# Performance work log

Hardware: AMD Instinct MI355X
Metric: run time of the kernel (lower is better)

Reference implementation:

```python
import jax, jax.numpy as jnp
import numpy as np

N_NODES = 50000
N_EDGES = 1600000
EMB_DIM = 128
HIDDEN = 128   # 2 * out_channels
OUT = 64       # out_channels


def setup_inputs() -> dict:
    key = jax.random.key(0)
    ks = jax.random.split(key, 8)
    x = jnp.arange(N_NODES, dtype=jnp.int64)
    edge_index = jax.random.randint(ks[0], (2, N_EDGES), 0, N_NODES, dtype=jnp.int64)
    emb = jax.random.normal(ks[1], (N_NODES, EMB_DIM), dtype=jnp.float32) * 0.02
    W1 = jax.random.normal(ks[2], (EMB_DIM, HIDDEN), dtype=jnp.float32) / np.sqrt(EMB_DIM).astype(np.float32)
    b1 = jax.random.normal(ks[3], (HIDDEN,), dtype=jnp.float32) * 0.01
    W_mu = jax.random.normal(ks[4], (HIDDEN, OUT), dtype=jnp.float32) / np.sqrt(HIDDEN).astype(np.float32)
    b_mu = jax.random.normal(ks[5], (OUT,), dtype=jnp.float32) * 0.01
    W_logvar = jax.random.normal(ks[6], (HIDDEN, OUT), dtype=jnp.float32) / np.sqrt(HIDDEN).astype(np.float32)
    b_logvar = jax.random.normal(ks[7], (OUT,), dtype=jnp.float32) * 0.01
    return {"x": x, "edge_index": edge_index, "emb": emb, "W1": W1, "b1": b1,
            "W_mu": W_mu, "b_mu": b_mu, "W_logvar": W_logvar, "b_logvar": b_logvar}


def _gcn_norm(edge_index, n_nodes):
    # PyG GCNConv default: add self-loops, symmetric normalization D^-1/2 A D^-1/2
    row, col = edge_index[0], edge_index[1]
    loop = jnp.arange(n_nodes, dtype=row.dtype)
    row = jnp.concatenate([row, loop])  # source nodes
    col = jnp.concatenate([col, loop])  # target nodes (aggregation index)
    deg = jax.ops.segment_sum(jnp.ones_like(col, dtype=jnp.float32), col, num_segments=n_nodes)
    dis = jnp.where(deg > 0, jax.lax.rsqrt(jnp.maximum(deg, 1.0)), 0.0)
    norm = dis[row] * dis[col]  # [E + N]
    return row, col, norm


def _gcn_conv(h, row, col, norm, W, b, n_nodes):
    h = h @ W                               # [N, out]
    msg = h[row] * norm[:, None]            # gather source feats, scale per edge
    out = jax.ops.segment_sum(msg, col, num_segments=n_nodes)  # scatter-add at targets
    return out + b


def reference(x, edge_index, emb, W1, b1, W_mu, b_mu, W_logvar, b_logvar):
    n_nodes = emb.shape[0]
    row, col, norm = _gcn_norm(edge_index, n_nodes)
    h = emb[x]                                                  # embedding lookup
    h = jax.nn.relu(_gcn_conv(h, row, col, norm, W1, b1, n_nodes))
    mu = _gcn_conv(h, row, col, norm, W_mu, b_mu, n_nodes)
    logvar = _gcn_conv(h, row, col, norm, W_logvar, b_logvar, n_nodes)
    return (mu, logvar)
```

## Files before the change

kernel.cpp:

```cpp
#include <hip/hip_runtime.h>
#include <hip/hip_bf16.h>

typedef unsigned int uint32;


__global__ __launch_bounds__(256)
void zero_cnt_kernel(uint32* __restrict__ cnt, int n) {
    int i = blockIdx.x * 256 + threadIdx.x;
    if (i < n) cnt[i] = 0u;
}

__global__ __launch_bounds__(256)
void count_kernel(const int* __restrict__ col, int n_edges, uint32* __restrict__ cnt) {
    int e = blockIdx.x * 256 + threadIdx.x;
    if (e < n_edges) atomicAdd(&cnt[col[e]], 1u);
}

__global__ __launch_bounds__(256)
void scan_blk_kernel(const uint32* __restrict__ cnt, uint32* __restrict__ partial,
                     uint32* __restrict__ blk_sums, int n) {
    __shared__ uint32 sh[256];
    int i = blockIdx.x * 256 + (int)threadIdx.x;
    uint32 v = (i < n) ? cnt[i] : 0u;
    sh[threadIdx.x] = v;
    __syncthreads();
    for (int off = 1; off < 256; off <<= 1) {
        uint32 t = (threadIdx.x >= (unsigned)off) ? sh[threadIdx.x - off] : 0u;
        __syncthreads();
        sh[threadIdx.x] += t;
        __syncthreads();
    }
    if (i < n) partial[i] = sh[threadIdx.x] - v;
    if (threadIdx.x == 255) blk_sums[blockIdx.x] = sh[255];
}

__global__ __launch_bounds__(1024)
void scan_sums_kernel(const uint32* __restrict__ blk_sums, uint32* __restrict__ blk_offs, int nb) {
    __shared__ uint32 sh[1024];
    uint32 v = ((int)threadIdx.x < nb) ? blk_sums[threadIdx.x] : 0u;
    sh[threadIdx.x] = v;
    __syncthreads();
    for (int off = 1; off < 1024; off <<= 1) {
        uint32 t = (threadIdx.x >= (unsigned)off) ? sh[threadIdx.x - off] : 0u;
        __syncthreads();
        sh[threadIdx.x] += t;
        __syncthreads();
    }
    if ((int)threadIdx.x < nb) blk_offs[threadIdx.x] = sh[threadIdx.x] - v;
}

__global__ __launch_bounds__(256)
void scan_add_kernel(const uint32* __restrict__ partial, const uint32* __restrict__ blk_offs,
                     const uint32* __restrict__ cnt, uint32* __restrict__ offs,
                     float* __restrict__ dis, uint32* __restrict__ cursor,
                     int n, int n_edges) {
    int i = blockIdx.x * 256 + (int)threadIdx.x;
    if (i < n) {
        offs[i] = partial[i] + blk_offs[blockIdx.x];
        dis[i] = rsqrtf((float)(cnt[i] + 1u));
        cursor[i] = 0u;
    }
    if (i == 0) offs[n] = (uint32)n_edges;
}

__global__ __launch_bounds__(256)
void fill_kernel(const int* __restrict__ row, const int* __restrict__ col, int n_edges,
                 const uint32* __restrict__ offs, uint32* __restrict__ cursor,
                 uint32* __restrict__ csr) {
    int e = blockIdx.x * 256 + threadIdx.x;
    if (e < n_edges) {
        int c = col[e];
        uint32 p = offs[c] + atomicAdd(&cursor[c], 1u);
        csr[p] = (uint32)row[e];
    }
}

static __device__ __forceinline__ uint32 f32_to_bf16_rne(float f) {
    uint32 u = __float_as_uint(f);
    return (u + 0x7fffu + ((u >> 16) & 1u)) >> 16;
}
static __device__ __forceinline__ float bf16_lo(uint32 v) {
    return __uint_as_float(v << 16);
}
static __device__ __forceinline__ float bf16_hi(uint32 v) {
    return __uint_as_float(v & 0xffff0000u);
}

__global__ __launch_bounds__(256)
void gemm_scale_kernel(const float* __restrict__ A, const int* __restrict__ gather,
                       const float* __restrict__ W0, const float* __restrict__ W1b,
                       int wstride, const float* __restrict__ dis,
                       uint32* __restrict__ out, int n_rows) {
    int grp = threadIdx.x >> 4;
    int c8  = (threadIdx.x & 15) * 8;
    int r0  = blockIdx.x * 64 + grp * 4;
    if (r0 >= n_rows) return;

    const float* wb = (c8 < 64) ? (W0 + c8) : (W1b + (c8 - 64));

    const float* ap[4];
    #pragma unroll
    for (int i = 0; i < 4; i++) {
        int r = r0 + i;
        if (r > n_rows - 1) r = n_rows - 1;
        int ra = gather ? gather[r] : r;
        ap[i] = A + (size_t)ra * 128;
    }

    float acc[4][8];
    #pragma unroll
    for (int i = 0; i < 4; i++)
        #pragma unroll
        for (int j = 0; j < 8; j++) acc[i][j] = 0.f;

    for (int k = 0; k < 128; k += 4) {
        float4 av[4];
        #pragma unroll
        for (int i = 0; i < 4; i++) av[i] = *(const float4*)(ap[i] + k);

        const float* w = wb + (size_t)k * wstride;
        #pragma unroll
        for (int kk = 0; kk < 4; kk++) {
            float4 w0 = *(const float4*)(w);
            float4 w1 = *(const float4*)(w + 4);
            #pragma unroll
            for (int i = 0; i < 4; i++) {
                float s = (kk == 0) ? av[i].x : (kk == 1) ? av[i].y
                        : (kk == 2) ? av[i].z : av[i].w;
                acc[i][0] = fmaf(s, w0.x, acc[i][0]);
                acc[i][1] = fmaf(s, w0.y, acc[i][1]);
                acc[i][2] = fmaf(s, w0.z, acc[i][2]);
                acc[i][3] = fmaf(s, w0.w, acc[i][3]);
                acc[i][4] = fmaf(s, w1.x, acc[i][4]);
                acc[i][5] = fmaf(s, w1.y, acc[i][5]);
                acc[i][6] = fmaf(s, w1.z, acc[i][6]);
                acc[i][7] = fmaf(s, w1.w, acc[i][7]);
            }
            w += wstride;
        }
    }

    #pragma unroll
    for (int i = 0; i < 4; i++) {
        int r = r0 + i;
        if (r < n_rows) {
            float d = dis[r];
            uint4 pk;
            pk.x = f32_to_bf16_rne(d * acc[i][0]) | (f32_to_bf16_rne(d * acc[i][1]) << 16);
            pk.y = f32_to_bf16_rne(d * acc[i][2]) | (f32_to_bf16_rne(d * acc[i][3]) << 16);
            pk.z = f32_to_bf16_rne(d * acc[i][4]) | (f32_to_bf16_rne(d * acc[i][5]) << 16);
            pk.w = f32_to_bf16_rne(d * acc[i][6]) | (f32_to_bf16_rne(d * acc[i][7]) << 16);
            *(uint4*)(out + (size_t)r * 64 + (c8 >> 1)) = pk;
        }
    }
}

__global__ __launch_bounds__(256)
void agg_relu_kernel(const uint32* __restrict__ hs, const uint32* __restrict__ offs,
                     const uint32* __restrict__ csr, const float* __restrict__ dis,
                     const float* __restrict__ bias, float* __restrict__ out, int n_nodes) {
    int wid = (blockIdx.x * 256 + (int)threadIdx.x) >> 6;
    int lane = threadIdx.x & 63;
    if (wid >= n_nodes) return;

    uint32 sv = hs[(size_t)wid * 64 + lane];
    float ax = bf16_lo(sv), ay = bf16_hi(sv);
    int beg = (int)offs[wid], end = (int)offs[wid + 1];

    int j = beg;
    for (; j + 8 <= end; j += 8) {
        uint32 e0 = csr[j],     e1 = csr[j + 1], e2 = csr[j + 2], e3 = csr[j + 3];
        uint32 e4 = csr[j + 4], e5 = csr[j + 5], e6 = csr[j + 6], e7 = csr[j + 7];
        uint32 v0 = hs[(size_t)e0 * 64 + lane];
        uint32 v1 = hs[(size_t)e1 * 64 + lane];
        uint32 v2 = hs[(size_t)e2 * 64 + lane];
        uint32 v3 = hs[(size_t)e3 * 64 + lane];
        uint32 v4 = hs[(size_t)e4 * 64 + lane];
        uint32 v5 = hs[(size_t)e5 * 64 + lane];
        uint32 v6 = hs[(size_t)e6 * 64 + lane];
        uint32 v7 = hs[(size_t)e7 * 64 + lane];
        float sx = ((bf16_lo(v0) + bf16_lo(v1)) + (bf16_lo(v2) + bf16_lo(v3)))
                 + ((bf16_lo(v4) + bf16_lo(v5)) + (bf16_lo(v6) + bf16_lo(v7)));
        float sy = ((bf16_hi(v0) + bf16_hi(v1)) + (bf16_hi(v2) + bf16_hi(v3)))
                 + ((bf16_hi(v4) + bf16_hi(v5)) + (bf16_hi(v6) + bf16_hi(v7)));
        ax += sx; ay += sy;
    }
    for (; j < end; ++j) {
        uint32 v = hs[(size_t)csr[j] * 64 + lane];
        ax += bf16_lo(v); ay += bf16_hi(v);
    }

    float d = dis[wid];
    float2 b = ((const float2*)bias)[lane];
    float2 o;
    o.x = fmaxf(fmaf(d, ax, b.x), 0.f);
    o.y = fmaxf(fmaf(d, ay, b.y), 0.f);
    ((float2*)out)[(size_t)wid * 64 + lane] = o;
}

__global__ __launch_bounds__(256)
void agg_out_kernel(const uint32* __restrict__ hs, const uint32* __restrict__ offs,
                    const uint32* __restrict__ csr, const float* __restrict__ dis,
                    const float* __restrict__ bmu, const float* __restrict__ blv,
                    float* __restrict__ out_mu, float* __restrict__ out_lv, int n_nodes) {
    int wid = (blockIdx.x * 256 + (int)threadIdx.x) >> 6;
    int lane = threadIdx.x & 63;
    if (wid >= n_nodes) return;

    uint32 sv = hs[(size_t)wid * 64 + lane];
    float ax = bf16_lo(sv), ay = bf16_hi(sv);
    int beg = (int)offs[wid], end = (int)offs[wid + 1];

    int j = beg;
    for (; j + 8 <= end; j += 8) {
        uint32 e0 = csr[j],     e1 = csr[j + 1], e2 = csr[j + 2], e3 = csr[j + 3];
        uint32 e4 = csr[j + 4], e5 = csr[j + 5], e6 = csr[j + 6], e7 = csr[j + 7];
        uint32 v0 = hs[(size_t)e0 * 64 + lane];
        uint32 v1 = hs[(size_t)e1 * 64 + lane];
        uint32 v2 = hs[(size_t)e2 * 64 + lane];
        uint32 v3 = hs[(size_t)e3 * 64 + lane];
        uint32 v4 = hs[(size_t)e4 * 64 + lane];
        uint32 v5 = hs[(size_t)e5 * 64 + lane];
        uint32 v6 = hs[(size_t)e6 * 64 + lane];
        uint32 v7 = hs[(size_t)e7 * 64 + lane];
        float sx = ((bf16_lo(v0) + bf16_lo(v1)) + (bf16_lo(v2) + bf16_lo(v3)))
                 + ((bf16_lo(v4) + bf16_lo(v5)) + (bf16_lo(v6) + bf16_lo(v7)));
        float sy = ((bf16_hi(v0) + bf16_hi(v1)) + (bf16_hi(v2) + bf16_hi(v3)))
                 + ((bf16_hi(v4) + bf16_hi(v5)) + (bf16_hi(v6) + bf16_hi(v7)));
        ax += sx; ay += sy;
    }
    for (; j < end; ++j) {
        uint32 v = hs[(size_t)csr[j] * 64 + lane];
        ax += bf16_lo(v); ay += bf16_hi(v);
    }

    float d = dis[wid];
    if (lane < 32) {
        float2 b = ((const float2*)bmu)[lane];
        float2 o = make_float2(fmaf(d, ax, b.x), fmaf(d, ay, b.y));
        ((float2*)out_mu)[(size_t)wid * 32 + lane] = o;
    } else {
        int l2 = lane - 32;
        float2 b = ((const float2*)blv)[l2];
        float2 o = make_float2(fmaf(d, ax, b.x), fmaf(d, ay, b.y));
        ((float2*)out_lv)[(size_t)wid * 32 + l2] = o;
    }
}


extern "C" void kernel_launch(void* const* d_in, const int* in_sizes, int n_in,
                              void* d_out, int out_size, void* d_ws, size_t ws_size,
                              hipStream_t stream) {
    const int*   x   = (const int*)d_in[0];
    const int*   ei  = (const int*)d_in[1];
    const float* emb = (const float*)d_in[2];
    const float* W1  = (const float*)d_in[3];
    const float* b1  = (const float*)d_in[4];
    const float* Wmu = (const float*)d_in[5];
    const float* bmu = (const float*)d_in[6];
    const float* Wlv = (const float*)d_in[7];
    const float* blv = (const float*)d_in[8];

    int n_nodes = in_sizes[0];
    int n_edges = in_sizes[1] / 2;
    const int* row = ei;
    const int* col = ei + n_edges;

    char* wp = (char*)d_ws;
    auto carve = [&wp](size_t bytes) -> char* {
        char* p = wp;
        wp += (bytes + 255) & ~(size_t)255;
        return p;
    };
    int nb = (n_nodes + 255) / 256;

    uint32* cnt     = (uint32*)carve((size_t)n_nodes * 4);
    uint32* cursor  = (uint32*)carve((size_t)n_nodes * 4);
    uint32* offs    = (uint32*)carve(((size_t)n_nodes + 1) * 4);
    uint32* partial = (uint32*)carve((size_t)n_nodes * 4);
    uint32* bsums   = (uint32*)carve((size_t)nb * 4);
    uint32* boffs   = (uint32*)carve((size_t)nb * 4);
    float*  dis     = (float*) carve((size_t)n_nodes * 4);
    uint32* csr     = (uint32*)carve((size_t)n_edges * 4);
    uint32* bufA    = (uint32*)carve((size_t)n_nodes * 64 * 4);
    float*  bufB    = (float*) carve((size_t)n_nodes * 128 * 4);

    int gb_e = (n_edges + 255) / 256;

    hipLaunchKernelGGL(zero_cnt_kernel, dim3(nb), dim3(256), 0, stream, cnt, n_nodes);
    hipLaunchKernelGGL(count_kernel, dim3(gb_e), dim3(256), 0, stream, col, n_edges, cnt);
    hipLaunchKernelGGL(scan_blk_kernel, dim3(nb), dim3(256), 0, stream, cnt, partial, bsums, n_nodes);
    hipLaunchKernelGGL(scan_sums_kernel, dim3(1), dim3(1024), 0, stream, bsums, boffs, nb);
    hipLaunchKernelGGL(scan_add_kernel, dim3(nb), dim3(256), 0, stream,
                       partial, boffs, cnt, offs, dis, cursor, n_nodes, n_edges);
    hipLaunchKernelGGL(fill_kernel, dim3(gb_e), dim3(256), 0, stream, row, col, n_edges, offs, cursor, csr);

    int gemm_blocks = (n_nodes + 63) / 64;
    int agg_blocks  = (n_nodes + 3) / 4;

    hipLaunchKernelGGL(gemm_scale_kernel, dim3(gemm_blocks), dim3(256), 0, stream,
                       emb, x, W1, W1 + 64, 128, dis, bufA, n_nodes);
    hipLaunchKernelGGL(agg_relu_kernel, dim3(agg_blocks), dim3(256), 0, stream,
                       bufA, offs, csr, dis, b1, bufB, n_nodes);

    hipLaunchKernelGGL(gemm_scale_kernel, dim3(gemm_blocks), dim3(256), 0, stream,
                       bufB, (const int*)nullptr, Wmu, Wlv, 64, dis, bufA, n_nodes);

    float* out_mu = (float*)d_out;
    float* out_lv = out_mu + (size_t)n_nodes * 64;
    hipLaunchKernelGGL(agg_out_kernel, dim3(agg_blocks), dim3(256), 0, stream,
                       bufA, offs, csr, dis, bmu, blv, out_mu, out_lv, n_nodes);
}
```

Before: 495.8 us.

## Fuse CSR fill with first GEMM and move source degree scaling into aggregation

Takes the source-side dis scaling out of the GEMM epilogue, so the first GEMM no longer depends on the degree scan. That GEMM is then merged with the CSR fill into one interleaved launch, with one GEMM block for every eight fill blocks, so the two independent workloads overlap on the GPU. In exchange, the aggregation kernels now do an extra gather of dis[e] per edge and use serial FMA chains in place of tree sums. This adds per-edge memory traffic and a longer dependency chain in the hot gather loop.

```diff
diff --git a/kernel.cpp b/kernel.cpp
--- a/kernel.cpp
+++ b/kernel.cpp
@@ -63,18 +63,6 @@
     if (i == 0) offs[n] = (uint32)n_edges;
 }
 
-__global__ __launch_bounds__(256)
-void fill_kernel(const int* __restrict__ row, const int* __restrict__ col, int n_edges,
-                 const uint32* __restrict__ offs, uint32* __restrict__ cursor,
-                 uint32* __restrict__ csr) {
-    int e = blockIdx.x * 256 + threadIdx.x;
-    if (e < n_edges) {
-        int c = col[e];
-        uint32 p = offs[c] + atomicAdd(&cursor[c], 1u);
-        csr[p] = (uint32)row[e];
-    }
-}
-
 static __device__ __forceinline__ uint32 f32_to_bf16_rne(float f) {
     uint32 u = __float_as_uint(f);
     return (u + 0x7fffu + ((u >> 16) & 1u)) >> 16;
@@ -86,14 +74,13 @@
     return __uint_as_float(v & 0xffff0000u);
 }
 
-__global__ __launch_bounds__(256)
-void gemm_scale_kernel(const float* __restrict__ A, const int* __restrict__ gather,
-                       const float* __restrict__ W0, const float* __restrict__ W1b,
-                       int wstride, const float* __restrict__ dis,
-                       uint32* __restrict__ out, int n_rows) {
+static __device__ __forceinline__
+void gemm_body(int gbid, const float* __restrict__ A, const int* __restrict__ gather,
+               const float* __restrict__ W0, const float* __restrict__ W1b,
+               int wstride, uint32* __restrict__ out, int n_rows) {
     int grp = threadIdx.x >> 4;
     int c8  = (threadIdx.x & 15) * 8;
-    int r0  = blockIdx.x * 64 + grp * 4;
+    int r0  = gbid * 64 + grp * 4;
     if (r0 >= n_rows) return;
 
     const float* wb = (c8 < 64) ? (W0 + c8) : (W1b + (c8 - 64));
@@ -144,15 +131,47 @@
     for (int i = 0; i < 4; i++) {
         int r = r0 + i;
         if (r < n_rows) {
-            float d = dis[r];
             uint4 pk;
-            pk.x = f32_to_bf16_rne(d * acc[i][0]) | (f32_to_bf16_rne(d * acc[i][1]) << 16);
-            pk.y = f32_to_bf16_rne(d * acc[i][2]) | (f32_to_bf16_rne(d * acc[i][3]) << 16);
-            pk.z = f32_to_bf16_rne(d * acc[i][4]) | (f32_to_bf16_rne(d * acc[i][5]) << 16);
-            pk.w = f32_to_bf16_rne(d * acc[i][6]) | (f32_to_bf16_rne(d * acc[i][7]) << 16);
+            pk.x = f32_to_bf16_rne(acc[i][0]) | (f32_to_bf16_rne(acc[i][1]) << 16);
+            pk.y = f32_to_bf16_rne(acc[i][2]) | (f32_to_bf16_rne(acc[i][3]) << 16);
+            pk.z = f32_to_bf16_rne(acc[i][4]) | (f32_to_bf16_rne(acc[i][5]) << 16);
+            pk.w = f32_to_bf16_rne(acc[i][6]) | (f32_to_bf16_rne(acc[i][7]) << 16);
             *(uint4*)(out + (size_t)r * 64 + (c8 >> 1)) = pk;
         }
     }
+}
+
+__global__ __launch_bounds__(256)
+void fill_gemm_kernel(const int* __restrict__ row, const int* __restrict__ col,
+                      int n_edges, const uint32* __restrict__ offs,
+                      uint32* __restrict__ cursor, uint32* __restrict__ csr,
+                      const float* __restrict__ A, const int* __restrict__ gather,
+                      const float* __restrict__ W0, const float* __restrict__ W1b,
+                      int wstride, uint32* __restrict__ out, int n_rows,
+                      int n_gemm_blocks) {
+    int bid = blockIdx.x;
+    int q = bid / 9, r = bid % 9;
+    bool is_gemm = (r == 0) && (q < n_gemm_blocks);
+    if (is_gemm) {
+        gemm_body(q, A, gather, W0, W1b, wstride, out, n_rows);
+    } else {
+        int before = q + (r ? 1 : 0);
+        if (before > n_gemm_blocks) before = n_gemm_blocks;
+        int fid = bid - before;
+        int e = fid * 256 + (int)threadIdx.x;
+        if (e < n_edges) {
+            int c = col[e];
+            uint32 p = offs[c] + atomicAdd(&cursor[c], 1u);
+            csr[p] = (uint32)row[e];
+        }
+    }
+}
+
+__global__ __launch_bounds__(256)
+void gemm_kernel(const float* __restrict__ A,
+                 const float* __restrict__ W0, const float* __restrict__ W1b,
+                 int wstride, uint32* __restrict__ out, int n_rows) {
+    gemm_body(blockIdx.x, A, (const int*)nullptr, W0, W1b, wstride, out, n_rows);
 }
 
 __global__ __launch_bounds__(256)
@@ -163,14 +182,17 @@
     int lane = threadIdx.x & 63;
     if (wid >= n_nodes) return;
 
+    float dv = dis[wid];
     uint32 sv = hs[(size_t)wid * 64 + lane];
-    float ax = bf16_lo(sv), ay = bf16_hi(sv);
+    float ax = dv * bf16_lo(sv), ay = dv * bf16_hi(sv);
     int beg = (int)offs[wid], end = (int)offs[wid + 1];
 
     int j = beg;
     for (; j + 8 <= end; j += 8) {
         uint32 e0 = csr[j],     e1 = csr[j + 1], e2 = csr[j + 2], e3 = csr[j + 3];
         uint32 e4 = csr[j + 4], e5 = csr[j + 5], e6 = csr[j + 6], e7 = csr[j + 7];
+        float d0 = dis[e0], d1 = dis[e1], d2 = dis[e2], d3 = dis[e3];
+        float d4 = dis[e4], d5 = dis[e5], d6 = dis[e6], d7 = dis[e7];
         uint32 v0 = hs[(size_t)e0 * 64 + lane];
         uint32 v1 = hs[(size_t)e1 * 64 + lane];
         uint32 v2 = hs[(size_t)e2 * 64 + lane];
@@ -179,22 +201,26 @@
         uint32 v5 = hs[(size_t)e5 * 64 + lane];
         uint32 v6 = hs[(size_t)e6 * 64 + lane];
         uint32 v7 = hs[(size_t)e7 * 64 + lane];
-        float sx = ((bf16_lo(v0) + bf16_lo(v1)) + (bf16_lo(v2) + bf16_lo(v3)))
-                 + ((bf16_lo(v4) + bf16_lo(v5)) + (bf16_lo(v6) + bf16_lo(v7)));
-        float sy = ((bf16_hi(v0) + bf16_hi(v1)) + (bf16_hi(v2) + bf16_hi(v3)))
-                 + ((bf16_hi(v4) + bf16_hi(v5)) + (bf16_hi(v6) + bf16_hi(v7)));
-        ax += sx; ay += sy;
+        ax = fmaf(d0, bf16_lo(v0), ax); ay = fmaf(d0, bf16_hi(v0), ay);
+        ax = fmaf(d1, bf16_lo(v1), ax); ay = fmaf(d1, bf16_hi(v1), ay);
+        ax = fmaf(d2, bf16_lo(v2), ax); ay = fmaf(d2, bf16_hi(v2), ay);
+        ax = fmaf(d3, bf16_lo(v3), ax); ay = fmaf(d3, bf16_hi(v3), ay);
+        ax = fmaf(d4, bf16_lo(v4), ax); ay = fmaf(d4, bf16_hi(v4), ay);
+        ax = fmaf(d5, bf16_lo(v5), ax); ay = fmaf(d5, bf16_hi(v5), ay);
+        ax = fmaf(d6, bf16_lo(v6), ax); ay = fmaf(d6, bf16_hi(v6), ay);
+        ax = fmaf(d7, bf16_lo(v7), ax); ay = fmaf(d7, bf16_hi(v7), ay);
     }
     for (; j < end; ++j) {
-        uint32 v = hs[(size_t)csr[j] * 64 + lane];
-        ax += bf16_lo(v); ay += bf16_hi(v);
-    }
-
-    float d = dis[wid];
+        uint32 e = csr[j];
+        float d = dis[e];
+        uint32 v = hs[(size_t)e * 64 + lane];
+        ax = fmaf(d, bf16_lo(v), ax); ay = fmaf(d, bf16_hi(v), ay);
+    }
+
     float2 b = ((const float2*)bias)[lane];
     float2 o;
-    o.x = fmaxf(fmaf(d, ax, b.x), 0.f);
-    o.y = fmaxf(fmaf(d, ay, b.y), 0.f);
+    o.x = fmaxf(fmaf(dv, ax, b.x), 0.f);
+    o.y = fmaxf(fmaf(dv, ay, b.y), 0.f);
     ((float2*)out)[(size_t)wid * 64 + lane] = o;
 }
 
@@ -207,14 +233,17 @@
     int lane = threadIdx.x & 63;
     if (wid >= n_nodes) return;
 
+    float dv = dis[wid];
     uint32 sv = hs[(size_t)wid * 64 + lane];
-    float ax = bf16_lo(sv), ay = bf16_hi(sv);
+    float ax = dv * bf16_lo(sv), ay = dv * bf16_hi(sv);
     int beg = (int)offs[wid], end = (int)offs[wid + 1];
 
     int j = beg;
     for (; j + 8 <= end; j += 8) {
         uint32 e0 = csr[j],     e1 = csr[j + 1], e2 = csr[j + 2], e3 = csr[j + 3];
         uint32 e4 = csr[j + 4], e5 = csr[j + 5], e6 = csr[j + 6], e7 = csr[j + 7];
+        float d0 = dis[e0], d1 = dis[e1], d2 = dis[e2], d3 = dis[e3];
+        float d4 = dis[e4], d5 = dis[e5], d6 = dis[e6], d7 = dis[e7];
         uint32 v0 = hs[(size_t)e0 * 64 + lane];
         uint32 v1 = hs[(size_t)e1 * 64 + lane];
         uint32 v2 = hs[(size_t)e2 * 64 + lane];
@@ -223,26 +252,30 @@
         uint32 v5 = hs[(size_t)e5 * 64 + lane];
         uint32 v6 = hs[(size_t)e6 * 64 + lane];
         uint32 v7 = hs[(size_t)e7 * 64 + lane];
-        float sx = ((bf16_lo(v0) + bf16_lo(v1)) + (bf16_lo(v2) + bf16_lo(v3)))
-                 + ((bf16_lo(v4) + bf16_lo(v5)) + (bf16_lo(v6) + bf16_lo(v7)));
-        float sy = ((bf16_hi(v0) + bf16_hi(v1)) + (bf16_hi(v2) + bf16_hi(v3)))
-                 + ((bf16_hi(v4) + bf16_hi(v5)) + (bf16_hi(v6) + bf16_hi(v7)));
-        ax += sx; ay += sy;
+        ax = fmaf(d0, bf16_lo(v0), ax); ay = fmaf(d0, bf16_hi(v0), ay);
+        ax = fmaf(d1, bf16_lo(v1), ax); ay = fmaf(d1, bf16_hi(v1), ay);
+        ax = fmaf(d2, bf16_lo(v2), ax); ay = fmaf(d2, bf16_hi(v2), ay);
+        ax = fmaf(d3, bf16_lo(v3), ax); ay = fmaf(d3, bf16_hi(v3), ay);
+        ax = fmaf(d4, bf16_lo(v4), ax); ay = fmaf(d4, bf16_hi(v4), ay);
+        ax = fmaf(d5, bf16_lo(v5), ax); ay = fmaf(d5, bf16_hi(v5), ay);
+        ax = fmaf(d6, bf16_lo(v6), ax); ay = fmaf(d6, bf16_hi(v6), ay);
+        ax = fmaf(d7, bf16_lo(v7), ax); ay = fmaf(d7, bf16_hi(v7), ay);
     }
     for (; j < end; ++j) {
-        uint32 v = hs[(size_t)csr[j] * 64 + lane];
-        ax += bf16_lo(v); ay += bf16_hi(v);
-    }
-
-    float d = dis[wid];
+        uint32 e = csr[j];
+        float d = dis[e];
+        uint32 v = hs[(size_t)e * 64 + lane];
+        ax = fmaf(d, bf16_lo(v), ax); ay = fmaf(d, bf16_hi(v), ay);
+    }
+
     if (lane < 32) {
         float2 b = ((const float2*)bmu)[lane];
-        float2 o = make_float2(fmaf(d, ax, b.x), fmaf(d, ay, b.y));
+        float2 o = make_float2(fmaf(dv, ax, b.x), fmaf(dv, ay, b.y));
         ((float2*)out_mu)[(size_t)wid * 32 + lane] = o;
     } else {
         int l2 = lane - 32;
         float2 b = ((const float2*)blv)[l2];
-        float2 o = make_float2(fmaf(d, ax, b.x), fmaf(d, ay, b.y));
+        float2 o = make_float2(fmaf(dv, ax, b.x), fmaf(dv, ay, b.y));
         ((float2*)out_lv)[(size_t)wid * 32 + l2] = o;
     }
 }
@@ -286,6 +319,8 @@
     float*  bufB    = (float*) carve((size_t)n_nodes * 128 * 4);
 
     int gb_e = (n_edges + 255) / 256;
+    int gemm_blocks = (n_nodes + 63) / 64;
+    int agg_blocks  = (n_nodes + 3) / 4;
 
     hipLaunchKernelGGL(zero_cnt_kernel, dim3(nb), dim3(256), 0, stream, cnt, n_nodes);
     hipLaunchKernelGGL(count_kernel, dim3(gb_e), dim3(256), 0, stream, col, n_edges, cnt);
@@ -293,18 +328,16 @@
     hipLaunchKernelGGL(scan_sums_kernel, dim3(1), dim3(1024), 0, stream, bsums, boffs, nb);
     hipLaunchKernelGGL(scan_add_kernel, dim3(nb), dim3(256), 0, stream,
                        partial, boffs, cnt, offs, dis, cursor, n_nodes, n_edges);
-    hipLaunchKernelGGL(fill_kernel, dim3(gb_e), dim3(256), 0, stream, row, col, n_edges, offs, cursor, csr);
-
-    int gemm_blocks = (n_nodes + 63) / 64;
-    int agg_blocks  = (n_nodes + 3) / 4;
-
-    hipLaunchKernelGGL(gemm_scale_kernel, dim3(gemm_blocks), dim3(256), 0, stream,
-                       emb, x, W1, W1 + 64, 128, dis, bufA, n_nodes);
+
+    hipLaunchKernelGGL(fill_gemm_kernel, dim3(gb_e + gemm_blocks), dim3(256), 0, stream,
+                       row, col, n_edges, offs, cursor, csr,
+                       emb, x, W1, W1 + 64, 128, bufA, n_nodes, gemm_blocks);
+
     hipLaunchKernelGGL(agg_relu_kernel, dim3(agg_blocks), dim3(256), 0, stream,
                        bufA, offs, csr, dis, b1, bufB, n_nodes);
 
-    hipLaunchKernelGGL(gemm_scale_kernel, dim3(gemm_blocks), dim3(256), 0, stream,
-                       bufB, (const int*)nullptr, Wmu, Wlv, 64, dis, bufA, n_nodes);
+    hipLaunchKernelGGL(gemm_kernel, dim3(gemm_blocks), dim3(256), 0, stream,
+                       bufB, Wmu, Wlv, 64, bufA, n_nodes);
 
     float* out_mu = (float*)d_out;
     float* out_lv = out_mu + (size_t)n_nodes * 64;
```

Result: faster. 466.3 us (-5.9%).
